# Kernel tuning notes

Hardware: AMD Instinct MI355X
Metric: run time of the kernel (lower is better)

## Reference

```python
import jax, jax.numpy as jnp
import numpy as np
import math

B, S, D, H, L, DFF, VS, VT = 4, 4096, 512, 8, 6, 2048, 69, 69
DK = D // H
NF = max(1, math.ceil(math.log(D)))  # 7
FEAT = 34
EPS = 1e-6


def gelu_approx(x):
    c = math.sqrt(2.0 / math.pi)
    return 0.5 * x * (1.0 + jnp.tanh(c * (x + 0.044715 * x ** 3)))


def layernorm(x, alpha, bias):
    # torch .std() is unbiased (n-1)
    mean = x.mean(axis=-1, keepdims=True)
    var = ((x - mean) ** 2).sum(axis=-1, keepdims=True) / (x.shape[-1] - 1)
    return alpha * (x - mean) / (jnp.sqrt(var) + EPS) + bias


def performer(x, Wq, Wk, Wv, Wo, omega):
    # Wq/Wk/Wv/Wo: [D, D] (torch Linear weight layout, y = x @ W.T)
    q = (x @ Wq.T).reshape(B, S, H, DK)
    k = (x @ Wk.T).reshape(B, S, H, DK)
    v = (x @ Wv.T).reshape(B, S, H, DK)
    qp = jnp.exp(-0.5 * jnp.einsum('bshd,fd->bshf', q, omega) ** 2)
    kp = jnp.exp(-0.5 * jnp.einsum('bshd,fd->bshf', k, omega) ** 2)
    qp = qp / (qp.sum(axis=-1, keepdims=True) + EPS)
    kp = kp / (kp.sum(axis=-1, keepdims=True) + EPS)
    K_cum = jnp.cumsum(kp, axis=1)                                   # [B,S,H,F]
    KV_cum = jnp.cumsum(kp[..., None] * v[..., None, :], axis=1)     # [B,S,H,F,DK]
    # block_size_h = block_size_w = 1 -> key_indices = arange(S) clamped
    key_idx = jnp.clip(jnp.arange(S), 0, S - 1)
    K_sel = K_cum[:, key_idx]
    KV_sel = KV_cum[:, key_idx]
    num = jnp.einsum('bshf,bshfd->bshd', qp, KV_sel)
    den = jnp.einsum('bshf,bshf->bsh', qp, K_sel)[..., None]
    out = (num / (den + EPS)).reshape(B, S, D)
    return out @ Wo.T


def pos_encoding():
    pos = jnp.arange(S, dtype=jnp.float32)[:, None]
    div = jnp.exp(jnp.arange(0, D, 2, dtype=jnp.float32) * (-math.log(10000.0) / D))
    pe = jnp.zeros((S, D), dtype=jnp.float32)
    pe = pe.at[:, 0::2].set(jnp.sin(pos * div))
    pe = pe.at[:, 1::2].set(jnp.cos(pos * div))
    return pe


def setup_inputs():
    key = jax.random.key(0)
    ks = jax.random.split(key, 16)
    sc = 0.02
    token_ids = jax.random.randint(ks[0], (B, S), 0, VS)
    id_embed = jax.random.normal(ks[1], (VS, D), jnp.float32) * sc
    feat_proj_w = jax.random.normal(ks[2], (D, FEAT), jnp.float32) * sc
    feature_table = jnp.zeros((VS, FEAT), jnp.float32)  # module's global feature_array is zeros
    product_mask = jnp.zeros((VS,), bool).at[jnp.arange(13, 57)].set(True)
    wq = jax.random.normal(ks[3], (L, D, D), jnp.float32) * sc
    wk = jax.random.normal(ks[4], (L, D, D), jnp.float32) * sc
    wv = jax.random.normal(ks[5], (L, D, D), jnp.float32) * sc
    wo = jax.random.normal(ks[6], (L, D, D), jnp.float32) * sc
    omega = jax.random.normal(ks[7], (L, NF, DK), jnp.float32) / math.sqrt(DK)
    ln1_a = jnp.ones((L, D)); ln1_b = jnp.zeros((L, D))
    ln2_a = jnp.ones((L, D)); ln2_b = jnp.zeros((L, D))
    w1 = jax.random.normal(ks[8], (L, DFF, D), jnp.float32) * sc
    b1 = jnp.zeros((L, DFF))
    w2 = jax.random.normal(ks[9], (L, D, DFF), jnp.float32) * sc
    b2 = jnp.zeros((L, D))
    fin_a = jnp.ones((D,)); fin_b = jnp.zeros((D,))
    proj_w = jax.random.normal(ks[10], (VT, D), jnp.float32) * sc
    proj_b = jnp.zeros((VT,))
    return dict(token_ids=token_ids, id_embed=id_embed, feat_proj_w=feat_proj_w,
                feature_table=feature_table, product_mask=product_mask,
                wq=wq, wk=wk, wv=wv, wo=wo, omega=omega,
                ln1_a=ln1_a, ln1_b=ln1_b, ln2_a=ln2_a, ln2_b=ln2_b,
                w1=w1, b1=b1, w2=w2, b2=b2, fin_a=fin_a, fin_b=fin_b,
                proj_w=proj_w, proj_b=proj_b)


def reference(token_ids, id_embed, feat_proj_w, feature_table, product_mask,
              wq, wk, wv, wo, omega, ln1_a, ln1_b, ln2_a, ln2_b,
              w1, b1, w2, b2, fin_a, fin_b, proj_w, proj_b):
    # SpecialPlusFeatureLookup: id embedding + (masked) projected product features
    id_vec = id_embed[token_ids]                                  # [B,S,D]
    feats = feature_table[token_ids] @ feat_proj_w.T              # [B,S,D]
    feat_vec = jnp.where(product_mask[token_ids][..., None], feats, 0.0)
    x = id_vec + feat_vec + pos_encoding()[None]
    for i in range(L):
        xn = layernorm(x, ln1_a[i], ln1_b[i])
        x = x + performer(xn, wq[i], wk[i], wv[i], wo[i], omega[i])
        xn2 = layernorm(x, ln2_a[i], ln2_b[i])
        ff = gelu_approx(xn2 @ w1[i].T + b1[i]) @ w2[i].T + b2[i]
        x = x + ff
    x = layernorm(x, fin_a, fin_b)
    return x @ proj_w.T + proj_b                                  # [B,S,VT]
```

## Files before the change

kernel.cpp:

```cpp
#include <hip/hip_runtime.h>
#include <hip/hip_bf16.h>
#include <math.h>

#define Bsz   4
#define Ssz   4096
#define Dsz   512
#define Hsz   8
#define Lsz   6
#define DFFsz 2048
#define VTsz  69
#define VSsz  69
#define DKsz  64
#define NFsz  7
#define FEATsz 34
#define EPSf  1e-6f
#define CSsz  32
#define NCsz  128
#define Msz   (Bsz*Ssz)
#define QKVN  1536

typedef __hip_bfloat16 bf16;
using bf16x8 = __attribute__((ext_vector_type(8))) __bf16;
using f32x4  = __attribute__((ext_vector_type(4))) float;

#define GLOAD16(gp, lp)                                                        \
  __builtin_amdgcn_global_load_lds(                                            \
      (const __attribute__((address_space(1))) unsigned int*)(gp),             \
      (__attribute__((address_space(3))) unsigned int*)(lp), 16, 0, 0)

__device__ __forceinline__ unsigned short f2bf_bits(float f) {
  unsigned int u = __float_as_uint(f);
  u += 0x7fffu + ((u >> 16) & 1u);
  return (unsigned short)(u >> 16);
}
__device__ __forceinline__ float gelu_f(float x) {
  const float c2 = 1.5957691216057308f;
  float u = c2 * (x + 0.044715f * x * x * x);
  return x / (1.0f + __expf(-u));
}

__global__ void detect_kernel(const unsigned int* __restrict__ p, int* __restrict__ flag) {
  if (threadIdx.x == 0 && blockIdx.x == 0) *flag = (p[0] == 0x3F800000u) ? 0 : 1;
}
__device__ __forceinline__ float load_as_f32(const void* p, int i, int flag) {
  if (flag == 0) return ((const float*)p)[i];
  unsigned int u = ((const unsigned short*)p)[i];
  return __uint_as_float(u << 16);
}
__global__ __launch_bounds__(256) void to_bf16_kernel(const void* __restrict__ in,
    unsigned short* __restrict__ out, int n, const int* __restrict__ flag) {
  int i = blockIdx.x * 256 + threadIdx.x;
  if (i >= n) return;
  if (*flag == 0) out[i] = f2bf_bits(((const float*)in)[i]);
  else            out[i] = ((const unsigned short*)in)[i];
}
__global__ __launch_bounds__(256) void to_f32_kernel(const void* __restrict__ in,
    float* __restrict__ out, int n, const int* __restrict__ flag) {
  int i = blockIdx.x * 256 + threadIdx.x;
  if (i >= n) return;
  out[i] = load_as_f32(in, i, *flag);
}
__global__ __launch_bounds__(256) void pack_qkv_kernel(const void* __restrict__ wq,
    const void* __restrict__ wk, const void* __restrict__ wv,
    unsigned short* __restrict__ dst, const int* __restrict__ flag) {
  int gid = blockIdx.x * 256 + threadIdx.x;
  int l = gid / (QKVN * Dsz);
  int rem = gid - l * (QKVN * Dsz);
  int r = rem >> 9;
  int d = rem & 511;
  const void* src = (r < 512) ? wq : (r < 1024) ? wk : wv;
  int rr = (r < 512) ? r : (r < 1024) ? r - 512 : r - 1024;
  float v = load_as_f32(src, l * (Dsz * Dsz) + rr * Dsz + d, *flag);
  dst[gid] = f2bf_bits(v);
}
__global__ __launch_bounds__(256) void pad_pw_kernel(const void* __restrict__ pw,
    const void* __restrict__ pb, unsigned short* __restrict__ pwp,
    float* __restrict__ pbp, const int* __restrict__ flag) {
  int gid = blockIdx.x * 256 + threadIdx.x;
  int n = gid >> 9, d = gid & 511;
  float v = (n < VTsz) ? load_as_f32(pw, n * Dsz + d, *flag) : 0.0f;
  pwp[gid] = f2bf_bits(v);
  if (gid < 128) pbp[gid] = (gid < VTsz) ? load_as_f32(pb, gid, *flag) : 0.0f;
}

__global__ __launch_bounds__(256) void tokvec_kernel(const float* __restrict__ idE,
    const float* __restrict__ fpw, const float* __restrict__ ftab,
    float* __restrict__ tokvec) {
  int gid = blockIdx.x * 256 + threadIdx.x;
  int tk = gid >> 9, d = gid & 511;
  float fs = 0.0f;
  #pragma unroll
  for (int j = 0; j < FEATsz; ++j)
    fs += ftab[tk * FEATsz + j] * fpw[d * FEATsz + j];
  tokvec[gid] = idE[gid] + fs;
}
__global__ __launch_bounds__(256) void embed_kernel(const int* __restrict__ tok,
    const float* __restrict__ tokvec, float* __restrict__ x) {
  int gid = blockIdx.x * 256 + threadIdx.x;
  int p = gid & 255, bs = gid >> 8;
  int tk = tok[bs];
  float div = __expf(-0.035977892078f * (float)p);
  float sv, cv;
  __sincosf((float)(bs & (Ssz - 1)) * div, &sv, &cv);
  float2 tv = ((const float2*)tokvec)[tk * 256 + p];
  float2 o; o.x = tv.x + sv; o.y = tv.y + cv;
  ((float2*)x)[gid] = o;
}

__global__ __launch_bounds__(256) void ln_kernel(const float* __restrict__ x,
    const float* __restrict__ ga, const float* __restrict__ gb, bf16* __restrict__ out) {
  __shared__ float red[8];
  const int row = blockIdx.x;
  const int t = threadIdx.x;
  float2 v = ((const float2*)(x + (size_t)row * Dsz))[t];
  float s = v.x + v.y;
  #pragma unroll
  for (int o = 32; o > 0; o >>= 1) s += __shfl_down(s, o, 64);
  if ((t & 63) == 0) red[t >> 6] = s;
  __syncthreads();
  if (t == 0) red[4] = (red[0] + red[1] + red[2] + red[3]) * (1.0f / Dsz);
  __syncthreads();
  const float mean = red[4];
  float d0 = v.x - mean, d1 = v.y - mean;
  float q = d0 * d0 + d1 * d1;
  #pragma unroll
  for (int o = 32; o > 0; o >>= 1) q += __shfl_down(q, o, 64);
  __syncthreads();
  if ((t & 63) == 0) red[t >> 6] = q;
  __syncthreads();
  if (t == 0) red[4] = red[0] + red[1] + red[2] + red[3];
  __syncthreads();
  const float inv = 1.0f / (sqrtf(red[4] * (1.0f / (Dsz - 1))) + EPSf);
  float2 gav = ((const float2*)ga)[t];
  float2 gbv = ((const float2*)gb)[t];
  ushort2 o2;
  o2.x = f2bf_bits(gav.x * (d0 * inv) + gbv.x);
  o2.y = f2bf_bits(gav.y * (d1 * inv) + gbv.y);
  ((ushort2*)out)[(size_t)row * 256 + t] = o2;
}

template<bool BIAS, bool GELUACT, int OUT>
__global__ __launch_bounds__(256) void gemm_bt(
    const bf16* __restrict__ A, const bf16* __restrict__ Bw,
    const float* __restrict__ bias, bf16* __restrict__ Obf,
    float* __restrict__ Of, int N, int K) {
  __shared__ __attribute__((aligned(128))) char lds[32768];
  const int t = threadIdx.x;
  const int lane = t & 63;
  const int wm = t >> 7;
  const int wn = (t >> 6) & 1;
  const int gx = gridDim.x;
  const int nwg = gx * gridDim.y;
  int f = blockIdx.y * gx + blockIdx.x;
  f = ((f & 7) * (nwg >> 3)) + (f >> 3);
  const int tileN = (f % gx) * 128;
  const int tileM = (f / gx) * 128;

  f32x4 acc[4][4];
  f32x4 zz = {0.f, 0.f, 0.f, 0.f};
  #pragma unroll
  for (int i = 0; i < 4; ++i)
    #pragma unroll
    for (int j = 0; j < 4; ++j) acc[i][j] = zz;

  const int r_st = t >> 3;
  const int kgs  = (t & 7) ^ (r_st & 7);
  const bf16* gA0 = A  + (size_t)(tileM + r_st) * K + kgs * 8;
  const bf16* gB0 = Bw + (size_t)(tileN + r_st) * K + kgs * 8;
  const int rowA = (wm * 64 + (lane & 15)) << 7;
  const int rowB = 16384 + ((wn * 64 + (lane & 15)) << 7);
  const int xo0 = (((lane >> 4) ^ (lane & 7)) << 4);
  const int xo1 = (((4 + (lane >> 4)) ^ (lane & 7)) << 4);

  for (int kt = 0; kt < K; kt += 64) {
    __syncthreads();
    #pragma unroll
    for (int it = 0; it < 4; ++it) {
      GLOAD16(gA0 + (size_t)(it * 32) * K + kt, lds +         it * 4096 + t * 16);
      GLOAD16(gB0 + (size_t)(it * 32) * K + kt, lds + 16384 + it * 4096 + t * 16);
    }
    __syncthreads();
    #pragma unroll
    for (int ks = 0; ks < 2; ++ks) {
      const int xo = ks ? xo1 : xo0;
      bf16x8 af[4], bfv[4];
      #pragma unroll
      for (int mi = 0; mi < 4; ++mi)
        af[mi] = *(const bf16x8*)(lds + rowA + mi * 2048 + xo);
      #pragma unroll
      for (int ni = 0; ni < 4; ++ni)
        bfv[ni] = *(const bf16x8*)(lds + rowB + ni * 2048 + xo);
      #pragma unroll
      for (int mi = 0; mi < 4; ++mi)
        #pragma unroll
        for (int ni = 0; ni < 4; ++ni)
          acc[mi][ni] = __builtin_amdgcn_mfma_f32_16x16x32_bf16(
              af[mi], bfv[ni], acc[mi][ni], 0, 0, 0);
    }
  }

  if (OUT == 0) {
    __syncthreads();
    #pragma unroll
    for (int mi = 0; mi < 4; ++mi)
      #pragma unroll
      for (int ni = 0; ni < 4; ++ni) {
        const int col = wn * 64 + ni * 16 + (lane & 15);
        const float bv = BIAS ? bias[tileN + col] : 0.0f;
        #pragma unroll
        for (int j = 0; j < 4; ++j) {
          const int row = wm * 64 + mi * 16 + ((lane >> 4) << 2) + j;
          float vv = acc[mi][ni][j] + bv;
          if (GELUACT) vv = gelu_f(vv);
          *(unsigned short*)(lds + (size_t)row * 256 +
                             ((col * 2) ^ (((row >> 2) & 7) << 5))) = f2bf_bits(vv);
        }
      }
    __syncthreads();
    #pragma unroll
    for (int p = 0; p < 8; ++p) {
      const int flat = p * 4096 + t * 16;
      const int row = flat >> 8, cb = flat & 255;
      uint4 v = *(const uint4*)(lds + (size_t)row * 256 + (cb ^ (((row >> 2) & 7) << 5)));
      *(uint4*)((char*)(Obf + (size_t)(tileM + row) * N + tileN) + cb) = v;
    }
  } else {
    const int rBase = tileM + wm * 64 + ((lane >> 4) << 2);
    const int cBase = tileN + wn * 64 + (lane & 15);
    #pragma unroll
    for (int ni = 0; ni < 4; ++ni) {
      const int col = cBase + ni * 16;
      const float bv = BIAS ? bias[col] : 0.0f;
      #pragma unroll
      for (int mi = 0; mi < 4; ++mi) {
        #pragma unroll
        for (int j = 0; j < 4; ++j) {
          const int rr2 = rBase + mi * 16 + j;
          float vv = acc[mi][ni][j] + bv;
          if (GELUACT) vv = gelu_f(vv);
          if (OUT == 1) Of[(size_t)rr2 * N + col] += vv;
          else          Of[(size_t)rr2 * N + col] = vv;
        }
      }
    }
  }
}

__global__ __launch_bounds__(256) void featmap2_kernel(const bf16* __restrict__ qkv,
    const float* __restrict__ om, float* __restrict__ qp, float* __restrict__ kp) {
  const int idx = blockIdx.x * 256 + threadIdx.x;
  const int row = idx >> 3, h = idx & 7;
  const bf16x8* qr = (const bf16x8*)(qkv + (size_t)row * QKVN + h * DKsz);
  const bf16x8* kr = (const bf16x8*)(qkv + (size_t)row * QKVN + 512 + h * DKsz);
  float qv[DKsz], kv[DKsz];
  #pragma unroll
  for (int j = 0; j < 8; ++j) {
    bf16x8 a = qr[j], b = kr[j];
    #pragma unroll
    for (int u = 0; u < 8; ++u) { qv[j * 8 + u] = (float)a[u]; kv[j * 8 + u] = (float)b[u]; }
  }
  float tq[NFsz], tk[NFsz];
  float sq = 0.f, sk = 0.f;
  #pragma unroll
  for (int ff = 0; ff < NFsz; ++ff) {
    const float* orow = om + ff * DKsz;
    float dq = 0.f, dk = 0.f;
    #pragma unroll
    for (int u = 0; u < DKsz; ++u) { dq += qv[u] * orow[u]; dk += kv[u] * orow[u]; }
    float eq = __expf(-0.5f * dq * dq), ek = __expf(-0.5f * dk * dk);
    tq[ff] = eq; sq += eq;
    tk[ff] = ek; sk += ek;
  }
  float iq = 1.0f / (sq + EPSf), ik = 1.0f / (sk + EPSf);
  #pragma unroll
  for (int ff = 0; ff < NFsz; ++ff) {
    qp[(size_t)idx * NFsz + ff] = tq[ff] * iq;
    kp[(size_t)idx * NFsz + ff] = tk[ff] * ik;
  }
}

__global__ __launch_bounds__(256) void pscan_partial(
    const float* __restrict__ kp, const bf16* __restrict__ qkv,
    float* __restrict__ kvS, float* __restrict__ kS) {
  __shared__ float skp[4][CSsz * NFsz];
  const int w = threadIdx.x >> 6;
  const int lane = threadIdx.x & 63;
  const int cid = blockIdx.x * 4 + w;
  const int c = cid & (NCsz - 1);
  const int bh = cid >> 7;
  const int h = bh & (Hsz - 1);
  const int b = bh >> 3;
  const int s0 = c * CSsz;
  const size_t kpbase = ((size_t)(b * Ssz + s0) * Hsz + h) * NFsz;
  for (int i = lane; i < CSsz * NFsz; i += 64) {
    int s = i / NFsz, f2 = i - s * NFsz;
    skp[w][i] = kp[kpbase + (size_t)s * (Hsz * NFsz) + f2];
  }
  float st[NFsz], ks[NFsz];
  #pragma unroll
  for (int ff = 0; ff < NFsz; ++ff) { st[ff] = 0.f; ks[ff] = 0.f; }
  const bf16* vb = qkv + (size_t)(b * Ssz + s0) * QKVN + 1024 + h * DKsz + lane;
  for (int s = 0; s < CSsz; ++s) {
    const float vv = __bfloat162float(vb[(size_t)s * QKVN]);
    #pragma unroll
    for (int ff = 0; ff < NFsz; ++ff) {
      float kf = skp[w][s * NFsz + ff];
      st[ff] += kf * vv;
      ks[ff] += kf;
    }
  }
  float* kvo = kvS + (size_t)cid * (NFsz * DKsz);
  #pragma unroll
  for (int ff = 0; ff < NFsz; ++ff) kvo[ff * DKsz + lane] = st[ff];
  if (lane < NFsz) {
    float val = 0.f;
    #pragma unroll
    for (int ff = 0; ff < NFsz; ++ff) val = (lane == ff) ? ks[ff] : val;
    kS[(size_t)cid * NFsz + lane] = val;
  }
}

__global__ __launch_bounds__(512) void pscan_scan(float* __restrict__ kvS, float* __restrict__ kS) {
  const int bh = blockIdx.x;
  const int comp = threadIdx.x;
  if (comp < NFsz * DKsz) {
    float run = 0.f;
    size_t base = (size_t)bh * NCsz * (NFsz * DKsz) + comp;
    #pragma unroll 8
    for (int c = 0; c < NCsz; ++c) {
      size_t ix = base + (size_t)c * (NFsz * DKsz);
      float tv = kvS[ix]; kvS[ix] = run; run += tv;
    }
  } else if (comp < NFsz * DKsz + NFsz) {
    int ff = comp - NFsz * DKsz;
    float run = 0.f;
    #pragma unroll 8
    for (int c = 0; c < NCsz; ++c) {
      size_t ix = (size_t)bh * NCsz * NFsz + ff + (size_t)c * NFsz;
      float tv = kS[ix]; kS[ix] = run; run += tv;
    }
  }
}

__global__ __launch_bounds__(256) void pscan_out(
    const float* __restrict__ qp, const float* __restrict__ kp,
    const bf16* __restrict__ qkv, const float* __restrict__ kvS,
    const float* __restrict__ kS, bf16* __restrict__ attn) {
  __shared__ float skp[4][CSsz * NFsz];
  __shared__ float sqp[4][CSsz * NFsz];
  const int w = threadIdx.x >> 6;
  const int lane = threadIdx.x & 63;
  const int cid = blockIdx.x * 4 + w;
  const int c = cid & (NCsz - 1);
  const int bh = cid >> 7;
  const int h = bh & (Hsz - 1);
  const int b = bh >> 3;
  const int s0 = c * CSsz;
  const size_t pbase = ((size_t)(b * Ssz + s0) * Hsz + h) * NFsz;
  for (int i = lane; i < CSsz * NFsz; i += 64) {
    int s = i / NFsz, f2 = i - s * NFsz;
    size_t gix = pbase + (size_t)s * (Hsz * NFsz) + f2;
    skp[w][i] = kp[gix];
    sqp[w][i] = qp[gix];
  }
  float kvst[NFsz], kst[NFsz];
  #pragma unroll
  for (int ff = 0; ff < NFsz; ++ff) kvst[ff] = kvS[(size_t)cid * (NFsz * DKsz) + ff * DKsz + lane];
  #pragma unroll
  for (int ff = 0; ff < NFsz; ++ff) kst[ff] = kS[(size_t)cid * NFsz + ff];
  const bf16* vb = qkv + (size_t)(b * Ssz + s0) * QKVN + 1024 + h * DKsz + lane;
  bf16* ob = attn + (size_t)(b * Ssz + s0) * Dsz + h * DKsz + lane;
  for (int s = 0; s < CSsz; ++s) {
    const float vv = __bfloat162float(vb[(size_t)s * QKVN]);
    float num = 0.f, den = 0.f;
    #pragma unroll
    for (int ff = 0; ff < NFsz; ++ff) {
      float kf = skp[w][s * NFsz + ff];
      kvst[ff] += kf * vv;
      kst[ff]  += kf;
      float qf = sqp[w][s * NFsz + ff];
      num += qf * kvst[ff];
      den += qf * kst[ff];
    }
    ob[(size_t)s * Dsz] = __float2bfloat16(num / (den + EPSf));
  }
}

__global__ __launch_bounds__(256) void proj_finish(const float* __restrict__ pt,
    void* __restrict__ out, const int* __restrict__ flag) {
  int gid = blockIdx.x * 256 + threadIdx.x;
  if (gid >= Msz * VTsz) return;
  int m = gid / VTsz, n = gid - m * VTsz;
  float r = pt[(size_t)m * 128 + n];
  if (*flag == 0) ((float*)out)[gid] = r;
  else            ((unsigned short*)out)[gid] = f2bf_bits(r);
}

extern "C" void kernel_launch(void* const* d_in, const int* in_sizes, int n_in,
                              void* d_out, int out_size, void* d_ws, size_t ws_size,
                              hipStream_t stream) {
  (void)in_sizes; (void)n_in; (void)out_size; (void)ws_size;
  const int* tok = (const int*)d_in[0];

  char* ws = (char*)d_ws;
  size_t off = 0;
  auto take = [&](size_t bytes) -> char* {
    char* p = ws + off; off += (bytes + 255) & ~(size_t)255; return p;
  };
  float* x    = (float*)take((size_t)Msz * Dsz * 4);
  bf16*  xn   = (bf16*) take((size_t)Msz * Dsz * 2);
  bf16*  hbuf = (bf16*) take((size_t)Msz * DFFsz * 2);
  bf16*  qkv  = (bf16*) take((size_t)Msz * QKVN * 2);
  float* qp   = (float*)take((size_t)Msz * Hsz * NFsz * 4);
  float* kp   = (float*)take((size_t)Msz * Hsz * NFsz * 4);
  float* kvS  = (float*)take((size_t)Bsz * Hsz * NCsz * NFsz * DKsz * 4);
  float* kS   = (float*)take((size_t)Bsz * Hsz * NCsz * NFsz * 4);
  float* ptmp = (float*)take((size_t)Msz * 128 * 4);
  bf16*  wqkvb= (bf16*) take((size_t)Lsz * QKVN * Dsz * 2);
  bf16*  wob  = (bf16*) take((size_t)Lsz * Dsz * Dsz * 2);
  bf16*  w1b  = (bf16*) take((size_t)Lsz * DFFsz * Dsz * 2);
  bf16*  w2b  = (bf16*) take((size_t)Lsz * Dsz * DFFsz * 2);
  bf16*  pwp  = (bf16*) take((size_t)128 * Dsz * 2);
  float* pbp  = (float*)take((size_t)128 * 4);
  float* tokv = (float*)take((size_t)VSsz * Dsz * 4);
  float* idEF = (float*)take((size_t)VSsz * Dsz * 4);
  float* fpwF = (float*)take((size_t)Dsz * FEATsz * 4);
  float* ftabF= (float*)take((size_t)VSsz * FEATsz * 4);
  float* omF  = (float*)take((size_t)Lsz * NFsz * DKsz * 4);
  float* l1aF = (float*)take((size_t)Lsz * Dsz * 4);
  float* l1bF = (float*)take((size_t)Lsz * Dsz * 4);
  float* l2aF = (float*)take((size_t)Lsz * Dsz * 4);
  float* l2bF = (float*)take((size_t)Lsz * Dsz * 4);
  float* b1F  = (float*)take((size_t)Lsz * DFFsz * 4);
  float* b2F  = (float*)take((size_t)Lsz * Dsz * 4);
  float* finaF= (float*)take((size_t)Dsz * 4);
  float* finbF= (float*)take((size_t)Dsz * 4);
  int*   flag = (int*)  take(16);

  detect_kernel<<<1, 1, 0, stream>>>((const unsigned int*)d_in[10], flag);

  auto cvtB = [&](const void* src, bf16* dst, int n) {
    to_bf16_kernel<<<(n + 255) / 256, 256, 0, stream>>>(src, (unsigned short*)dst, n, flag);
  };
  auto cvtF = [&](const void* src, float* dst, int n) {
    to_f32_kernel<<<(n + 255) / 256, 256, 0, stream>>>(src, dst, n, flag);
  };
  pack_qkv_kernel<<<(Lsz * QKVN * Dsz) / 256, 256, 0, stream>>>(
      d_in[5], d_in[6], d_in[7], (unsigned short*)wqkvb, flag);
  cvtB(d_in[8],  wob, Lsz * Dsz * Dsz);
  cvtB(d_in[14], w1b, Lsz * DFFsz * Dsz);
  cvtB(d_in[16], w2b, Lsz * Dsz * DFFsz);
  pad_pw_kernel<<<(128 * Dsz) / 256, 256, 0, stream>>>(d_in[20], d_in[21],
      (unsigned short*)pwp, pbp, flag);
  cvtF(d_in[1],  idEF, VSsz * Dsz);
  cvtF(d_in[2],  fpwF, Dsz * FEATsz);
  cvtF(d_in[3],  ftabF, VSsz * FEATsz);
  cvtF(d_in[9],  omF,  Lsz * NFsz * DKsz);
  cvtF(d_in[10], l1aF, Lsz * Dsz);
  cvtF(d_in[11], l1bF, Lsz * Dsz);
  cvtF(d_in[12], l2aF, Lsz * Dsz);
  cvtF(d_in[13], l2bF, Lsz * Dsz);
  cvtF(d_in[15], b1F,  Lsz * DFFsz);
  cvtF(d_in[17], b2F,  Lsz * Dsz);
  cvtF(d_in[18], finaF, Dsz);
  cvtF(d_in[19], finbF, Dsz);

  tokvec_kernel<<<(VSsz * Dsz) / 256, 256, 0, stream>>>(idEF, fpwF, ftabF, tokv);
  embed_kernel<<<Msz, 256, 0, stream>>>(tok, tokv, x);

  dim3 gQKV(QKVN / 128, Msz / 128);
  dim3 gO  (Dsz  / 128, Msz / 128);
  dim3 gFF1(DFFsz/ 128, Msz / 128);
  dim3 gFF2(Dsz  / 128, Msz / 128);
  dim3 gPRJ(1, Msz / 128);
  for (int i = 0; i < Lsz; ++i) {
    ln_kernel<<<Msz, 256, 0, stream>>>(x, l1aF + i * Dsz, l1bF + i * Dsz, xn);
    gemm_bt<false, false, 0><<<gQKV, 256, 0, stream>>>(
        xn, wqkvb + (size_t)i * QKVN * Dsz, nullptr, qkv, nullptr, QKVN, Dsz);
    featmap2_kernel<<<Msz * Hsz / 256, 256, 0, stream>>>(
        qkv, omF + (size_t)i * NFsz * DKsz, qp, kp);
    pscan_partial<<<Bsz * Hsz * NCsz / 4, 256, 0, stream>>>(kp, qkv, kvS, kS);
    pscan_scan<<<Bsz * Hsz, 512, 0, stream>>>(kvS, kS);
    pscan_out<<<Bsz * Hsz * NCsz / 4, 256, 0, stream>>>(qp, kp, qkv, kvS, kS, hbuf);
    gemm_bt<false, false, 1><<<gO, 256, 0, stream>>>(
        hbuf, wob + (size_t)i * Dsz * Dsz, nullptr, nullptr, x, Dsz, Dsz);
    ln_kernel<<<Msz, 256, 0, stream>>>(x, l2aF + i * Dsz, l2bF + i * Dsz, xn);
    gemm_bt<true, true, 0><<<gFF1, 256, 0, stream>>>(
        xn, w1b + (size_t)i * DFFsz * Dsz, b1F + i * DFFsz, hbuf, nullptr, DFFsz, Dsz);
    gemm_bt<true, false, 1><<<gFF2, 256, 0, stream>>>(
        hbuf, w2b + (size_t)i * Dsz * DFFsz, b2F + i * Dsz, nullptr, x, Dsz, DFFsz);
  }
  ln_kernel<<<Msz, 256, 0, stream>>>(x, finaF, finbF, xn);
  gemm_bt<true, false, 2><<<gPRJ, 256, 0, stream>>>(
      xn, pwp, pbp, nullptr, ptmp, 128, Dsz);
  proj_finish<<<(Msz * VTsz + 255) / 256, 256, 0, stream>>>(ptmp, d_out, flag);
}
```

Baseline: 1.783 ms.

## Fuse feature map into scan kernels, template GEMM K, batch conversion launches

Removes the separate featmap kernel and its qp/kp buffers. The random-feature projection and normalisation are now recomputed from qkv inside pscan_partial and pscan_out, with two lanes per row and a shuffle reduction writing into LDS. The GEMM takes K as a template parameter and fully unrolls the K loop. The many small weight and parameter conversion launches are merged into two batched kernels. This trades redundant feature-map compute on k (done in both scan passes) for less global traffic and fewer launches, and the full unroll may raise code size and register pressure.

New measurement: 1.692 ms. 5.1% less time.

```diff
diff --git a/kernel.cpp b/kernel.cpp
--- a/kernel.cpp
+++ b/kernel.cpp
@@ -47,19 +47,60 @@
   unsigned int u = ((const unsigned short*)p)[i];
   return __uint_as_float(u << 16);
 }
-__global__ __launch_bounds__(256) void to_bf16_kernel(const void* __restrict__ in,
-    unsigned short* __restrict__ out, int n, const int* __restrict__ flag) {
+
+#define OFF_OM    0
+#define OFF_L1A   2688
+#define OFF_L1B   5760
+#define OFF_L2A   8832
+#define OFF_L2B   11904
+#define OFF_B1    14976
+#define OFF_B2    27264
+#define OFF_FINA  30336
+#define OFF_FINB  30848
+#define OFF_IDE   31360
+#define OFF_FPW   66688
+#define OFF_FTAB  84096
+#define SMALL_TOT 86442
+__global__ __launch_bounds__(256) void cvt_smalls_kernel(
+    const void* om, const void* l1a, const void* l1b, const void* l2a,
+    const void* l2b, const void* b1, const void* b2, const void* fina,
+    const void* finb, const void* idE, const void* fpw, const void* ftab,
+    float* __restrict__ dst, const int* __restrict__ flag) {
   int i = blockIdx.x * 256 + threadIdx.x;
-  if (i >= n) return;
-  if (*flag == 0) out[i] = f2bf_bits(((const float*)in)[i]);
-  else            out[i] = ((const unsigned short*)in)[i];
-}
-__global__ __launch_bounds__(256) void to_f32_kernel(const void* __restrict__ in,
-    float* __restrict__ out, int n, const int* __restrict__ flag) {
+  if (i >= SMALL_TOT) return;
+  const void* src; int off;
+  if      (i < OFF_L1A)  { src = om;   off = OFF_OM; }
+  else if (i < OFF_L1B)  { src = l1a;  off = OFF_L1A; }
+  else if (i < OFF_L2A)  { src = l1b;  off = OFF_L1B; }
+  else if (i < OFF_L2B)  { src = l2a;  off = OFF_L2A; }
+  else if (i < OFF_B1)   { src = l2b;  off = OFF_L2B; }
+  else if (i < OFF_B2)   { src = b1;   off = OFF_B1; }
+  else if (i < OFF_FINA) { src = b2;   off = OFF_B2; }
+  else if (i < OFF_FINB) { src = fina; off = OFF_FINA; }
+  else if (i < OFF_IDE)  { src = finb; off = OFF_FINB; }
+  else if (i < OFF_FPW)  { src = idE;  off = OFF_IDE; }
+  else if (i < OFF_FTAB) { src = fpw;  off = OFF_FPW; }
+  else                   { src = ftab; off = OFF_FTAB; }
+  dst[i] = load_as_f32(src, i - off, *flag);
+}
+
+#define WO_N  (Lsz*Dsz*Dsz)
+#define W1_N  (Lsz*DFFsz*Dsz)
+#define W2_N  (Lsz*Dsz*DFFsz)
+#define W3_TOT (WO_N + W1_N + W2_N)
+__global__ __launch_bounds__(256) void cvt_w3_kernel(const void* wo,
+    const void* w1, const void* w2, unsigned short* __restrict__ dst,
+    const int* __restrict__ flag) {
   int i = blockIdx.x * 256 + threadIdx.x;
-  if (i >= n) return;
-  out[i] = load_as_f32(in, i, *flag);
-}
+  if (i >= W3_TOT) return;
+  const void* src; int off;
+  if      (i < WO_N)        { src = wo; off = 0; }
+  else if (i < WO_N + W1_N) { src = w1; off = WO_N; }
+  else                      { src = w2; off = WO_N + W1_N; }
+  if (*flag == 0) dst[i] = f2bf_bits(((const float*)src)[i - off]);
+  else            dst[i] = ((const unsigned short*)src)[i - off];
+}
+
 __global__ __launch_bounds__(256) void pack_qkv_kernel(const void* __restrict__ wq,
     const void* __restrict__ wk, const void* __restrict__ wv,
     unsigned short* __restrict__ dst, const int* __restrict__ flag) {
@@ -139,11 +180,11 @@
   ((ushort2*)out)[(size_t)row * 256 + t] = o2;
 }
 
-template<bool BIAS, bool GELUACT, int OUT>
+template<int KT, bool BIAS, bool GELUACT, int OUT>
 __global__ __launch_bounds__(256) void gemm_bt(
     const bf16* __restrict__ A, const bf16* __restrict__ Bw,
     const float* __restrict__ bias, bf16* __restrict__ Obf,
-    float* __restrict__ Of, int N, int K) {
+    float* __restrict__ Of, int N) {
   __shared__ __attribute__((aligned(128))) char lds[32768];
   const int t = threadIdx.x;
   const int lane = t & 63;
@@ -165,19 +206,20 @@
 
   const int r_st = t >> 3;
   const int kgs  = (t & 7) ^ (r_st & 7);
-  const bf16* gA0 = A  + (size_t)(tileM + r_st) * K + kgs * 8;
-  const bf16* gB0 = Bw + (size_t)(tileN + r_st) * K + kgs * 8;
+  const bf16* gA0 = A  + (size_t)(tileM + r_st) * KT + kgs * 8;
+  const bf16* gB0 = Bw + (size_t)(tileN + r_st) * KT + kgs * 8;
   const int rowA = (wm * 64 + (lane & 15)) << 7;
   const int rowB = 16384 + ((wn * 64 + (lane & 15)) << 7);
   const int xo0 = (((lane >> 4) ^ (lane & 7)) << 4);
   const int xo1 = (((4 + (lane >> 4)) ^ (lane & 7)) << 4);
 
-  for (int kt = 0; kt < K; kt += 64) {
+  #pragma unroll
+  for (int kt = 0; kt < KT; kt += 64) {
     __syncthreads();
     #pragma unroll
     for (int it = 0; it < 4; ++it) {
-      GLOAD16(gA0 + (size_t)(it * 32) * K + kt, lds +         it * 4096 + t * 16);
-      GLOAD16(gB0 + (size_t)(it * 32) * K + kt, lds + 16384 + it * 4096 + t * 16);
+      GLOAD16(gA0 + (size_t)(it * 32) * KT + kt, lds +         it * 4096 + t * 16);
+      GLOAD16(gB0 + (size_t)(it * 32) * KT + kt, lds + 16384 + it * 4096 + t * 16);
     }
     __syncthreads();
     #pragma unroll
@@ -246,41 +288,37 @@
   }
 }
 
-__global__ __launch_bounds__(256) void featmap2_kernel(const bf16* __restrict__ qkv,
-    const float* __restrict__ om, float* __restrict__ qp, float* __restrict__ kp) {
-  const int idx = blockIdx.x * 256 + threadIdx.x;
-  const int row = idx >> 3, h = idx & 7;
-  const bf16x8* qr = (const bf16x8*)(qkv + (size_t)row * QKVN + h * DKsz);
-  const bf16x8* kr = (const bf16x8*)(qkv + (size_t)row * QKVN + 512 + h * DKsz);
-  float qv[DKsz], kv[DKsz];
-  #pragma unroll
-  for (int j = 0; j < 8; ++j) {
-    bf16x8 a = qr[j], b = kr[j];
-    #pragma unroll
-    for (int u = 0; u < 8; ++u) { qv[j * 8 + u] = (float)a[u]; kv[j * 8 + u] = (float)b[u]; }
-  }
-  float tq[NFsz], tk[NFsz];
-  float sq = 0.f, sk = 0.f;
+__device__ __forceinline__ void featrow_to_lds(const bf16* __restrict__ rowp,
+    const float* __restrict__ om, float* __restrict__ dst, int lane) {
+  const int srow = lane >> 1, half = lane & 1;
+  const bf16x8* r8 = (const bf16x8*)rowp;
+  float v[32];
+  #pragma unroll
+  for (int j = 0; j < 4; ++j) {
+    bf16x8 a = r8[j];
+    #pragma unroll
+    for (int u = 0; u < 8; ++u) v[j * 8 + u] = (float)a[u];
+  }
+  float tt[NFsz]; float ssum = 0.f;
   #pragma unroll
   for (int ff = 0; ff < NFsz; ++ff) {
-    const float* orow = om + ff * DKsz;
-    float dq = 0.f, dk = 0.f;
-    #pragma unroll
-    for (int u = 0; u < DKsz; ++u) { dq += qv[u] * orow[u]; dk += kv[u] * orow[u]; }
-    float eq = __expf(-0.5f * dq * dq), ek = __expf(-0.5f * dk * dk);
-    tq[ff] = eq; sq += eq;
-    tk[ff] = ek; sk += ek;
-  }
-  float iq = 1.0f / (sq + EPSf), ik = 1.0f / (sk + EPSf);
-  #pragma unroll
-  for (int ff = 0; ff < NFsz; ++ff) {
-    qp[(size_t)idx * NFsz + ff] = tq[ff] * iq;
-    kp[(size_t)idx * NFsz + ff] = tk[ff] * ik;
+    const float* orow = om + ff * DKsz + half * 32;
+    float d = 0.f;
+    #pragma unroll
+    for (int u = 0; u < 32; ++u) d += v[u] * orow[u];
+    d += __shfl_xor(d, 1, 64);
+    float e = __expf(-0.5f * d * d);
+    tt[ff] = e; ssum += e;
+  }
+  float inv = 1.0f / (ssum + EPSf);
+  if (half == 0) {
+    #pragma unroll
+    for (int ff = 0; ff < NFsz; ++ff) dst[srow * NFsz + ff] = tt[ff] * inv;
   }
 }
 
 __global__ __launch_bounds__(256) void pscan_partial(
-    const float* __restrict__ kp, const bf16* __restrict__ qkv,
+    const bf16* __restrict__ qkv, const float* __restrict__ om,
     float* __restrict__ kvS, float* __restrict__ kS) {
   __shared__ float skp[4][CSsz * NFsz];
   const int w = threadIdx.x >> 6;
@@ -291,11 +329,10 @@
   const int h = bh & (Hsz - 1);
   const int b = bh >> 3;
   const int s0 = c * CSsz;
-  const size_t kpbase = ((size_t)(b * Ssz + s0) * Hsz + h) * NFsz;
-  for (int i = lane; i < CSsz * NFsz; i += 64) {
-    int s = i / NFsz, f2 = i - s * NFsz;
-    skp[w][i] = kp[kpbase + (size_t)s * (Hsz * NFsz) + f2];
-  }
+  featrow_to_lds(qkv + (size_t)(b * Ssz + s0 + (lane >> 1)) * QKVN + 512
+                     + h * DKsz + (lane & 1) * 32,
+                 om, skp[w], lane);
+  asm volatile("s_waitcnt lgkmcnt(0)" ::: "memory");
   float st[NFsz], ks[NFsz];
   #pragma unroll
   for (int ff = 0; ff < NFsz; ++ff) { st[ff] = 0.f; ks[ff] = 0.f; }
@@ -343,9 +380,9 @@
 }
 
 __global__ __launch_bounds__(256) void pscan_out(
-    const float* __restrict__ qp, const float* __restrict__ kp,
-    const bf16* __restrict__ qkv, const float* __restrict__ kvS,
-    const float* __restrict__ kS, bf16* __restrict__ attn) {
+    const bf16* __restrict__ qkv, const float* __restrict__ om,
+    const float* __restrict__ kvS, const float* __restrict__ kS,
+    bf16* __restrict__ attn) {
   __shared__ float skp[4][CSsz * NFsz];
   __shared__ float sqp[4][CSsz * NFsz];
   const int w = threadIdx.x >> 6;
@@ -356,13 +393,11 @@
   const int h = bh & (Hsz - 1);
   const int b = bh >> 3;
   const int s0 = c * CSsz;
-  const size_t pbase = ((size_t)(b * Ssz + s0) * Hsz + h) * NFsz;
-  for (int i = lane; i < CSsz * NFsz; i += 64) {
-    int s = i / NFsz, f2 = i - s * NFsz;
-    size_t gix = pbase + (size_t)s * (Hsz * NFsz) + f2;
-    skp[w][i] = kp[gix];
-    sqp[w][i] = qp[gix];
-  }
+  const bf16* rowbase = qkv + (size_t)(b * Ssz + s0 + (lane >> 1)) * QKVN
+                            + h * DKsz + (lane & 1) * 32;
+  featrow_to_lds(rowbase,       om, sqp[w], lane);
+  featrow_to_lds(rowbase + 512, om, skp[w], lane);
+  asm volatile("s_waitcnt lgkmcnt(0)" ::: "memory");
   float kvst[NFsz], kst[NFsz];
   #pragma unroll
   for (int ff = 0; ff < NFsz; ++ff) kvst[ff] = kvS[(size_t)cid * (NFsz * DKsz) + ff * DKsz + lane];
@@ -411,59 +446,43 @@
   bf16*  xn   = (bf16*) take((size_t)Msz * Dsz * 2);
   bf16*  hbuf = (bf16*) take((size_t)Msz * DFFsz * 2);
   bf16*  qkv  = (bf16*) take((size_t)Msz * QKVN * 2);
-  float* qp   = (float*)take((size_t)Msz * Hsz * NFsz * 4);
-  float* kp   = (float*)take((size_t)Msz * Hsz * NFsz * 4);
   float* kvS  = (float*)take((size_t)Bsz * Hsz * NCsz * NFsz * DKsz * 4);
   float* kS   = (float*)take((size_t)Bsz * Hsz * NCsz * NFsz * 4);
   float* ptmp = (float*)take((size_t)Msz * 128 * 4);
   bf16*  wqkvb= (bf16*) take((size_t)Lsz * QKVN * Dsz * 2);
-  bf16*  wob  = (bf16*) take((size_t)Lsz * Dsz * Dsz * 2);
-  bf16*  w1b  = (bf16*) take((size_t)Lsz * DFFsz * Dsz * 2);
-  bf16*  w2b  = (bf16*) take((size_t)Lsz * Dsz * DFFsz * 2);
+  bf16*  w3   = (bf16*) take((size_t)W3_TOT * 2);
   bf16*  pwp  = (bf16*) take((size_t)128 * Dsz * 2);
   float* pbp  = (float*)take((size_t)128 * 4);
   float* tokv = (float*)take((size_t)VSsz * Dsz * 4);
-  float* idEF = (float*)take((size_t)VSsz * Dsz * 4);
-  float* fpwF = (float*)take((size_t)Dsz * FEATsz * 4);
-  float* ftabF= (float*)take((size_t)VSsz * FEATsz * 4);
-  float* omF  = (float*)take((size_t)Lsz * NFsz * DKsz * 4);
-  float* l1aF = (float*)take((size_t)Lsz * Dsz * 4);
-  float* l1bF = (float*)take((size_t)Lsz * Dsz * 4);
-  float* l2aF = (float*)take((size_t)Lsz * Dsz * 4);
-  float* l2bF = (float*)take((size_t)Lsz * Dsz * 4);
-  float* b1F  = (float*)take((size_t)Lsz * DFFsz * 4);
-  float* b2F  = (float*)take((size_t)Lsz * Dsz * 4);
-  float* finaF= (float*)take((size_t)Dsz * 4);
-  float* finbF= (float*)take((size_t)Dsz * 4);
+  float* smalls = (float*)take((size_t)SMALL_TOT * 4);
   int*   flag = (int*)  take(16);
 
+  bf16* wob = w3;
+  bf16* w1b = w3 + WO_N;
+  bf16* w2b = w3 + WO_N + W1_N;
+  float* omF  = smalls + OFF_OM;
+  float* l1aF = smalls + OFF_L1A;
+  float* l1bF = smalls + OFF_L1B;
+  float* l2aF = smalls + OFF_L2A;
+  float* l2bF = smalls + OFF_L2B;
+  float* b1F  = smalls + OFF_B1;
+  float* b2F  = smalls + OFF_B2;
+  float* finaF= smalls + OFF_FINA;
+  float* finbF= smalls + OFF_FINB;
+  float* idEF = smalls + OFF_IDE;
+  float* fpwF = smalls + OFF_FPW;
+  float* ftabF= smalls + OFF_FTAB;
+
   detect_kernel<<<1, 1, 0, stream>>>((const unsigned int*)d_in[10], flag);
-
-  auto cvtB = [&](const void* src, bf16* dst, int n) {
-    to_bf16_kernel<<<(n + 255) / 256, 256, 0, stream>>>(src, (unsigned short*)dst, n, flag);
-  };
-  auto cvtF = [&](const void* src, float* dst, int n) {
-    to_f32_kernel<<<(n + 255) / 256, 256, 0, stream>>>(src, dst, n, flag);
-  };
   pack_qkv_kernel<<<(Lsz * QKVN * Dsz) / 256, 256, 0, stream>>>(
       d_in[5], d_in[6], d_in[7], (unsigned short*)wqkvb, flag);
-  cvtB(d_in[8],  wob, Lsz * Dsz * Dsz);
-  cvtB(d_in[14], w1b, Lsz * DFFsz * Dsz);
-  cvtB(d_in[16], w2b, Lsz * Dsz * DFFsz);
+  cvt_w3_kernel<<<(W3_TOT + 255) / 256, 256, 0, stream>>>(
+      d_in[8], d_in[14], d_in[16], (unsigned short*)w3, flag);
+  cvt_smalls_kernel<<<(SMALL_TOT + 255) / 256, 256, 0, stream>>>(
+      d_in[9], d_in[10], d_in[11], d_in[12], d_in[13], d_in[15], d_in[17],
+      d_in[18], d_in[19], d_in[1], d_in[2], d_in[3], smalls, flag);
   pad_pw_kernel<<<(128 * Dsz) / 256, 256, 0, stream>>>(d_in[20], d_in[21],
       (unsigned short*)pwp, pbp, flag);
-  cvtF(d_in[1],  idEF, VSsz * Dsz);
-  cvtF(d_in[2],  fpwF, Dsz * FEATsz);
-  cvtF(d_in[3],  ftabF, VSsz * FEATsz);
-  cvtF(d_in[9],  omF,  Lsz * NFsz * DKsz);
-  cvtF(d_in[10], l1aF, Lsz * Dsz);
-  cvtF(d_in[11], l1bF, Lsz * Dsz);
-  cvtF(d_in[12], l2aF, Lsz * Dsz);
-  cvtF(d_in[13], l2bF, Lsz * Dsz);
-  cvtF(d_in[15], b1F,  Lsz * DFFsz);
-  cvtF(d_in[17], b2F,  Lsz * Dsz);
-  cvtF(d_in[18], finaF, Dsz);
-  cvtF(d_in[19], finbF, Dsz);
 
   tokvec_kernel<<<(VSsz * Dsz) / 256, 256, 0, stream>>>(idEF, fpwF, ftabF, tokv);
   embed_kernel<<<Msz, 256, 0, stream>>>(tok, tokv, x);
@@ -475,23 +494,23 @@
   dim3 gPRJ(1, Msz / 128);
   for (int i = 0; i < Lsz; ++i) {
     ln_kernel<<<Msz, 256, 0, stream>>>(x, l1aF + i * Dsz, l1bF + i * Dsz, xn);
-    gemm_bt<false, false, 0><<<gQKV, 256, 0, stream>>>(
-        xn, wqkvb + (size_t)i * QKVN * Dsz, nullptr, qkv, nullptr, QKVN, Dsz);
-    featmap2_kernel<<<Msz * Hsz / 256, 256, 0, stream>>>(
-        qkv, omF + (size_t)i * NFsz * DKsz, qp, kp);
-    pscan_partial<<<Bsz * Hsz * NCsz / 4, 256, 0, stream>>>(kp, qkv, kvS, kS);
+    gemm_bt<512, false, false, 0><<<gQKV, 256, 0, stream>>>(
+        xn, wqkvb + (size_t)i * QKVN * Dsz, nullptr, qkv, nullptr, QKVN);
+    pscan_partial<<<Bsz * Hsz * NCsz / 4, 256, 0, stream>>>(
+        qkv, omF + (size_t)i * NFsz * DKsz, kvS, kS);
     pscan_scan<<<Bsz * Hsz, 512, 0, stream>>>(kvS, kS);
-    pscan_out<<<Bsz * Hsz * NCsz / 4, 256, 0, stream>>>(qp, kp, qkv, kvS, kS, hbuf);
-    gemm_bt<false, false, 1><<<gO, 256, 0, stream>>>(
-        hbuf, wob + (size_t)i * Dsz * Dsz, nullptr, nullptr, x, Dsz, Dsz);
+    pscan_out<<<Bsz * Hsz * NCsz / 4, 256, 0, stream>>>(
+        qkv, omF + (size_t)i * NFsz * DKsz, kvS, kS, hbuf);
+    gemm_bt<512, false, false, 1><<<gO, 256, 0, stream>>>(
+        hbuf, wob + (size_t)i * Dsz * Dsz, nullptr, nullptr, x, Dsz);
     ln_kernel<<<Msz, 256, 0, stream>>>(x, l2aF + i * Dsz, l2bF + i * Dsz, xn);
-    gemm_bt<true, true, 0><<<gFF1, 256, 0, stream>>>(
-        xn, w1b + (size_t)i * DFFsz * Dsz, b1F + i * DFFsz, hbuf, nullptr, DFFsz, Dsz);
-    gemm_bt<true, false, 1><<<gFF2, 256, 0, stream>>>(
-        hbuf, w2b + (size_t)i * Dsz * DFFsz, b2F + i * Dsz, nullptr, x, Dsz, DFFsz);
+    gemm_bt<512, true, true, 0><<<gFF1, 256, 0, stream>>>(
+        xn, w1b + (size_t)i * DFFsz * Dsz, b1F + i * DFFsz, hbuf, nullptr, DFFsz);
+    gemm_bt<2048, true, false, 1><<<gFF2, 256, 0, stream>>>(
+        hbuf, w2b + (size_t)i * Dsz * DFFsz, b2F + i * Dsz, nullptr, x, Dsz);
   }
   ln_kernel<<<Msz, 256, 0, stream>>>(x, finaF, finbF, xn);
-  gemm_bt<true, false, 2><<<gPRJ, 256, 0, stream>>>(
-      xn, pwp, pbp, nullptr, ptmp, 128, Dsz);
+  gemm_bt<512, true, false, 2><<<gPRJ, 256, 0, stream>>>(
+      xn, pwp, pbp, nullptr, ptmp, 128);
   proj_finish<<<(Msz * VTsz + 255) / 256, 256, 0, stream>>>(ptmp, d_out, flag);
 }
```
